# Optimization experiments

Measured on AMD Instinct MI355X. Metric: run time of the kernel, lower is better.

The kernel has to match this reference:

```python
import jax, jax.numpy as jnp
import numpy as np

N, E, NS, NB = 25000, 400000, 4, 8
S0, V0 = 64, 32            # input: 64x0e + 32x1o
MS, MV = 96, 96            # message irreps: 96x0e + 96x1o
OS, OV = 128, 32           # post-linear_down/skip: (64+64)x0e + 32x1o
NIRR = S0 + V0             # node_feats.irreps.num_irreps = 96
AVG_NEIGH = 16.0
Y1 = float(np.sqrt(3.0 / (4.0 * np.pi)))  # integral-normalized l=1 SH coeff


def setup_inputs() -> dict:
    key = jax.random.key(0)
    k = jax.random.split(key, 15)
    return {
        'node_feats': jax.random.normal(k[0], (N, S0 + 3 * V0), jnp.float32),
        'vectors': jax.random.normal(k[1], (E, 3), jnp.float32),
        'rbf': jax.random.uniform(k[2], (E, NB), jnp.float32),
        'species': jax.random.randint(k[3], (N,), 0, NS, jnp.int32),
        'senders': jax.random.randint(k[4], (E,), 0, N, jnp.int32),
        'receivers': jax.random.randint(k[5], (E,), 0, N, jnp.int32),
        'W_up_s': jax.random.normal(k[6], (S0, S0), jnp.float32),
        'W_up_v': jax.random.normal(k[7], (V0, V0), jnp.float32),
        'W_mlp1': jax.random.normal(k[8], (NB, 64), jnp.float32),
        'W_mlp2': jax.random.normal(k[9], (64, 64), jnp.float32),
        'W_mlp3': jax.random.normal(k[10], (64, MS + MV), jnp.float32),
        'W_down_s': jax.random.normal(k[11], (MS, OS), jnp.float32),
        'W_down_v': jax.random.normal(k[12], (MV, OV), jnp.float32),
        'W_skip_s': jax.random.normal(k[13], (NS, S0, OS), jnp.float32),
        'W_skip_v': jax.random.normal(k[14], (NS, V0, OV), jnp.float32),
    }


def reference(node_feats, vectors, rbf, species, senders, receivers,
              W_up_s, W_up_v, W_mlp1, W_mlp2, W_mlp3,
              W_down_s, W_down_v, W_skip_s, W_skip_v):
    n = node_feats.shape[0]
    s = node_feats[:, :S0]                      # [N, 64]   0e
    v = node_feats[:, S0:].reshape(n, V0, 3)    # [N, 32,3] 1o

    # linear_up (per-irrep linear, 1/sqrt(fan_in) path normalization), then gather
    s_up = (s @ W_up_s) * (1.0 / jnp.sqrt(S0))
    v_up = jnp.einsum('nci,cd->ndi', v, W_up_v) * (1.0 / jnp.sqrt(V0))
    s_e = s_up[senders]                         # [E, 64]
    v_e = v_up[senders]                         # [E, 32, 3]

    # spherical harmonics l=1, normalize=True, 'integral' normalization
    y = Y1 * vectors / (jnp.linalg.norm(vectors, axis=-1, keepdims=True) + 1e-12)

    # tensor products filtered to output irreps + 0e
    tp_v = s_e[:, :, None] * y[:, None, :]                       # 0e x 1o -> 1o [E,64,3]
    tp_s = jnp.einsum('eci,ei->ec', v_e, y) * (1.0 / jnp.sqrt(3.0))  # 1o x 1o -> 0e [E,32]
    msg_s = jnp.concatenate([s_e, tp_s], axis=1)                 # [E, 96]
    msg_v = jnp.concatenate([v_e, tp_v], axis=1)                 # [E, 96, 3]

    # radial MLP -> per-edge, per-irrep mixing weights
    h = jax.nn.silu(rbf @ W_mlp1 * (1.0 / jnp.sqrt(NB)))
    h = jax.nn.silu(h @ W_mlp2 * (1.0 / 8.0))
    mix = h @ W_mlp3 * (1.0 / 8.0)                               # [E, 192]

    inv = 1.0 / NIRR
    msg_s = msg_s * mix[:, :MS] * inv
    msg_v = msg_v * (mix[:, MS:] * inv)[:, :, None]

    # scatter-sum to receivers, then normalize by sqrt(avg_num_neighbors)
    agg_s = jax.ops.segment_sum(msg_s, receivers, num_segments=n) / jnp.sqrt(AVG_NEIGH)
    agg_v = jax.ops.segment_sum(msg_v, receivers, num_segments=n) / jnp.sqrt(AVG_NEIGH)

    # linear_down to 128x0e + 32x1o
    out_s = agg_s @ W_down_s * (1.0 / jnp.sqrt(MS))
    out_v = jnp.einsum('nci,cd->ndi', agg_v, W_down_v) * (1.0 / jnp.sqrt(MV))

    # species-indexed skip connection (indexed linear)
    skip_s = jnp.einsum('nc,ncd->nd', s, W_skip_s[species]) * (1.0 / jnp.sqrt(S0))
    skip_v = jnp.einsum('nci,ncd->ndi', v, W_skip_v[species]) * (1.0 / jnp.sqrt(V0))

    f_s = out_s + skip_s                                         # [N, 128]
    f_v = out_v + skip_v                                         # [N, 32, 3]

    # equivariant gate: first 96 scalars activated, last 32 scalars gate the vectors
    act_s = jax.nn.silu(f_s[:, :OS - OV])
    gates = jax.nn.silu(f_s[:, OS - OV:])
    gated_v = f_v * gates[:, :, None]
    return jnp.concatenate([act_s, gated_v.reshape(n, OV * 3)], axis=1)  # [N, 192]
```

## Files before the change

### kernel.cpp

```cpp
#include <hip/hip_runtime.h>
#include <hip/hip_bf16.h>
#include <hip/hip_fp16.h>
#include <hip/hip_fp8.h>

#define NN 25000
#define EE 400000

#define SC_UP_S 0.125f
#define SC_UP_V 0.17677669529663689f
#define Y1C 0.48860251190291992f
#define SC_MLP1 0.35355339059327373f
#define SC_MLP2 0.125f
#define SC3 0.0013020833333333333f
#define INV_SQRT3 0.57735026918962584f
#define SC_DOWN 0.025515518153991442f
#define SC_SKIP_S 0.125f
#define SC_SKIP_V 0.17677669529663689f

typedef __attribute__((ext_vector_type(8))) short short8;
typedef __attribute__((ext_vector_type(4))) float f32x4;

#if defined(__has_builtin)
#if __has_builtin(__builtin_amdgcn_cvt_pk_fp8_f32)
#define HAS_HW_FP8_ENC 1
#endif
#if __has_builtin(__builtin_amdgcn_cvt_pk_f32_fp8)
#define HAS_HW_FP8_DEC 1
#endif
#endif
#ifndef HAS_HW_FP8_ENC
#define HAS_HW_FP8_ENC 0
#endif
#ifndef HAS_HW_FP8_DEC
#define HAS_HW_FP8_DEC 0
#endif

__device__ __forceinline__ float silu(float x) {
  return __fdividef(x, 1.f + __expf(-x));
}
__device__ __forceinline__ unsigned short f2bf(float f) {
  __hip_bfloat16 h = __float2bfloat16(f);
  return *reinterpret_cast<unsigned short*>(&h);
}
__device__ __forceinline__ float bf2f(unsigned short s) {
  return __uint_as_float(((unsigned)s) << 16);
}
__device__ __forceinline__ float bfe(short8 v, int idx) {
  return __uint_as_float(((unsigned)(unsigned short)v[idx]) << 16);
}
__device__ __forceinline__ unsigned packbf(float lo, float hi) {
  return ((unsigned)f2bf(hi) << 16) | (unsigned)f2bf(lo);
}
__device__ __forceinline__ unsigned char f2fp8_sw(float x) {
  __hip_fp8_e4m3 v(x);
  return (unsigned char)v.__x;
}
__device__ __forceinline__ unsigned f2fp8x2(float a, float b) {
#if HAS_HW_FP8_ENC
  return (unsigned)__builtin_amdgcn_cvt_pk_fp8_f32(a, b, 0, false);
#else
  return (unsigned)f2fp8_sw(a) | ((unsigned)f2fp8_sw(b) << 8);
#endif
}
__device__ __forceinline__ float fp82f_sw(unsigned b) {
  __hip_fp8_e4m3 t;
  t.__x = (__hip_fp8_storage_t)b;
  return (float)t;
}
__device__ __forceinline__ void fp8x4dec(unsigned w, float* o) {
#if HAS_HW_FP8_DEC
  auto lo = __builtin_amdgcn_cvt_pk_f32_fp8((int)w, false);
  auto hi = __builtin_amdgcn_cvt_pk_f32_fp8((int)w, true);
  o[0] = lo[0]; o[1] = lo[1]; o[2] = hi[0]; o[3] = hi[1];
#else
  o[0] = fp82f_sw(w & 0xFF);
  o[1] = fp82f_sw((w >> 8) & 0xFF);
  o[2] = fp82f_sw((w >> 16) & 0xFF);
  o[3] = fp82f_sw(w >> 24);
#endif
}

#define W_W1P 0
#define W_W2P 1024
#define W_W3B 3072
#define W_WDS 9216
#define W_WDV 15360
#define W_WSS 16896
#define W_WSV 33280
#define W_SUPB 35328
#define W_VUPB (W_SUPB + NN * 32)
#define W_DEG (W_VUPB + NN * 48)
#define W_PRE (W_DEG + NN)
#define W_CUR (W_PRE + NN + 8)
#define W_RNK (W_CUR + NN)
#define W_EDN (W_RNK + EE)
#define W_END (W_EDN + EE * 56)


__global__ __launch_bounds__(256) void transpose_weights(
    const float* __restrict__ W1, const float* __restrict__ W2,
    const float* __restrict__ W3, const float* __restrict__ Wds,
    const float* __restrict__ Wdv, const float* __restrict__ Wss,
    const float* __restrict__ Wsv, float* __restrict__ ws) {
  int t = blockIdx.x * 256 + threadIdx.x;
  int stride = gridDim.x * 256;
  unsigned short* W1p = (unsigned short*)(ws + W_W1P);
  unsigned short* W2p = (unsigned short*)(ws + W_W2P);
  unsigned short* W3b = (unsigned short*)(ws + W_W3B);
  unsigned short* Wdsb = (unsigned short*)(ws + W_WDS);
  unsigned short* Wdvb = (unsigned short*)(ws + W_WDV);
  unsigned short* Wssb = (unsigned short*)(ws + W_WSS);
  unsigned short* Wsvb = (unsigned short*)(ws + W_WSV);
  for (int i = t; i < 2048; i += stride) {
    int c = i >> 5, k = i & 31;
    W1p[i] = (k < 8) ? f2bf(W1[k * 64 + c] * SC_MLP1) : (unsigned short)0;
  }
  for (int i = t; i < 4096; i += stride) {
    int c = i >> 6, k = i & 63;
    W2p[i] = f2bf(W2[k * 64 + c] * SC_MLP2);
  }
  for (int i = t; i < 12288; i += stride) {
    int c = i >> 6, k = i & 63;
    float sc = (c >= 64 && c < 96) ? (SC3 * INV_SQRT3) : SC3;
    W3b[i] = f2bf(W3[k * 192 + c] * sc);
  }
  for (int i = t; i < 12288; i += stride) {
    int o = i / 96, k = i - 96 * o;
    Wdsb[i] = f2bf(Wds[k * 128 + o] * SC_DOWN);
  }
  for (int i = t; i < 3072; i += stride) {
    int o = i / 96, k = i - 96 * o;
    Wdvb[i] = f2bf(Wdv[k * 32 + o] * SC_DOWN);
  }
  for (int i = t; i < 32768; i += stride)
    Wssb[i] = f2bf(Wss[i] * SC_SKIP_S);
  for (int i = t; i < 4096; i += stride)
    Wsvb[i] = f2bf(Wsv[i] * SC_SKIP_V);
}

__global__ __launch_bounds__(256) void up_kernel(
    const float* __restrict__ nf, const float* __restrict__ Wus,
    const float* __restrict__ Wuv, unsigned short* __restrict__ s_upb,
    unsigned short* __restrict__ v_upb) {
  int n = blockIdx.x;
  int t = threadIdx.x;
  __shared__ float sv[160];
  if (t < 160) sv[t] = nf[n * 160 + t];
  __syncthreads();
  if (t < 64) {
    float a = 0.f;
#pragma unroll
    for (int k = 0; k < 64; k++) a += sv[k] * Wus[k * 64 + t];
    s_upb[n * 64 + t] = f2bf(a * SC_UP_S);
  } else if (t < 160) {
    int j = t - 64;
    int c = j / 3, i = j - 3 * c;
    float a = 0.f;
#pragma unroll
    for (int k = 0; k < 32; k++) a += sv[64 + k * 3 + i] * Wuv[k * 32 + c];
    v_upb[n * 96 + j] = f2bf(a * SC_UP_V);
  }
}

__global__ __launch_bounds__(256) void count_deg(
    const int* __restrict__ receivers, int* __restrict__ deg) {
  int e = blockIdx.x * 256 + threadIdx.x;
  if (e < EE) atomicAdd(&deg[receivers[e]], 1);
}

__global__ __launch_bounds__(1024) void scan_kernel(
    const int* __restrict__ deg, int* __restrict__ prefix,
    int* __restrict__ cursor) {
  __shared__ int waveSums[16];
  __shared__ int sCarry;
  int t = threadIdx.x;
  int lane = t & 63, wv = t >> 6;
  if (t == 0) sCarry = 0;
  __syncthreads();
  for (int base = 0; base < NN; base += 1024) {
    int i = base + t;
    int x = (i < NN) ? deg[i] : 0;
    int v = x;
#pragma unroll
    for (int d = 1; d < 64; d <<= 1) {
      int u = __shfl_up(v, d, 64);
      if (lane >= d) v += u;
    }
    if (lane == 63) waveSums[wv] = v;
    __syncthreads();
    if (wv == 0 && lane < 16) {
      int s = waveSums[lane];
#pragma unroll
      for (int d = 1; d < 16; d <<= 1) {
        int u = __shfl_up(s, d, 64);
        if (lane >= d) s += u;
      }
      waveSums[lane] = s;
    }
    __syncthreads();
    int waveOff = (wv == 0) ? 0 : waveSums[wv - 1];
    int incl = v + waveOff + sCarry;
    if (i < NN) {
      prefix[i] = incl - x;
      cursor[i] = incl - x;
    }
    __syncthreads();
    if (t == 1023) sCarry = incl;
    __syncthreads();
  }
  if (t == 0) prefix[NN] = sCarry;
}

__global__ __launch_bounds__(256) void rank_kernel(
    const int* __restrict__ receivers, int* __restrict__ cursor,
    int* __restrict__ rankArr) {
  int e = blockIdx.x * 256 + threadIdx.x;
  if (e < EE) {
    int r = receivers[e];
    rankArr[e] = atomicAdd(&cursor[r], 1);
  }
}

__global__ __launch_bounds__(256, 4) void edge_down7(
    const float* __restrict__ rbf, const float* __restrict__ vectors,
    const int* __restrict__ senders, const int* __restrict__ rankArr,
    const unsigned short* __restrict__ W1p,
    const unsigned short* __restrict__ W2p,
    const unsigned short* __restrict__ W3b,
    const unsigned short* __restrict__ Wdsb,
    const unsigned short* __restrict__ Wdvb,
    const unsigned short* __restrict__ s_upb,
    const unsigned short* __restrict__ v_upb,
    unsigned char* __restrict__ edown) {
  __shared__ unsigned short sMix[64 * 200];
  unsigned short* sH = sMix;
  __shared__ int sRank[64];

  int t = threadIdx.x;
  int pbase = blockIdx.x * 64;
  int lane = t & 63;
  int wv = t >> 6;
  int rl = lane & 15;
  int kgrp = lane >> 4;
  int arow = 16 * wv + rl;
  int crow = 16 * wv + kgrp * 4;

  union S8 { short8 v; unsigned u[4]; };

  if (t < 64) sRank[t] = rankArr[pbase + t];
  int eid = pbase + arow;
  int snd = senders[eid];
  const unsigned short* seb = s_upb + (size_t)snd * 64;
  const unsigned short* veb = v_upb + (size_t)snd * 96;
  short8 se0 = *(const short8*)&seb[kgrp * 8];
  short8 se1 = *(const short8*)&seb[32 + kgrp * 8];
  short8 ve0 = *(const short8*)&veb[24 * kgrp];
  short8 ve1 = *(const short8*)&veb[24 * kgrp + 8];
  short8 ve2 = *(const short8*)&veb[24 * kgrp + 16];
  float vx = vectors[(size_t)eid * 3 + 0];
  float vy = vectors[(size_t)eid * 3 + 1];
  float vz = vectors[(size_t)eid * 3 + 2];
  float nrm = sqrtf(vx * vx + vy * vy + vz * vz) + 1e-12f;
  float ysc = Y1C / nrm;
  float y0 = vx * ysc, y1 = vy * ysc, y2 = vz * ysc;

  S8 a1;
  a1.u[0] = a1.u[1] = a1.u[2] = a1.u[3] = 0u;
  if (kgrp == 0) {
    float4 ra = *(const float4*)(rbf + (size_t)eid * 8);
    float4 rb = *(const float4*)(rbf + (size_t)eid * 8 + 4);
    a1.u[0] = packbf(ra.x, ra.y);
    a1.u[1] = packbf(ra.z, ra.w);
    a1.u[2] = packbf(rb.x, rb.y);
    a1.u[3] = packbf(rb.z, rb.w);
  }
#pragma unroll
  for (int ct = 0; ct < 4; ct++) {
    short8 b = *(const short8*)&W1p[(ct * 16 + rl) * 32 + kgrp * 8];
    f32x4 acc = {0.f, 0.f, 0.f, 0.f};
    acc = __builtin_amdgcn_mfma_f32_16x16x32_bf16(a1.v, b, acc, 0, 0, 0);
#pragma unroll
    for (int rr = 0; rr < 4; rr++)
      sH[(crow + rr) * 72 + ct * 16 + rl] = f2bf(silu(acc[rr]));
  }

  {
    short8 a20 = *(const short8*)&sH[arow * 72 + kgrp * 8];
    short8 a21 = *(const short8*)&sH[arow * 72 + 32 + kgrp * 8];
    short8 b0s[4], b1s[4];
#pragma unroll
    for (int ct = 0; ct < 4; ct++) {
      const unsigned short* wb = &W2p[(ct * 16 + rl) * 64];
      b0s[ct] = *(const short8*)&wb[kgrp * 8];
      b1s[ct] = *(const short8*)&wb[32 + kgrp * 8];
    }
#pragma unroll
    for (int ct = 0; ct < 4; ct++) {
      f32x4 acc = {0.f, 0.f, 0.f, 0.f};
      acc = __builtin_amdgcn_mfma_f32_16x16x32_bf16(a20, b0s[ct], acc, 0, 0, 0);
      acc = __builtin_amdgcn_mfma_f32_16x16x32_bf16(a21, b1s[ct], acc, 0, 0, 0);
#pragma unroll
      for (int rr = 0; rr < 4; rr++)
        sH[(crow + rr) * 72 + ct * 16 + rl] = f2bf(silu(acc[rr]));
    }
  }

  short8 a30 = *(const short8*)&sH[arow * 72 + kgrp * 8];
  short8 a31 = *(const short8*)&sH[arow * 72 + 32 + kgrp * 8];
  __syncthreads();
  {
#pragma unroll
    for (int half = 0; half < 2; half++) {
      short8 b0s[6], b1s[6];
#pragma unroll
      for (int j = 0; j < 6; j++) {
        int cc = (half * 6 + j) * 16 + rl;
        const unsigned short* wb = &W3b[cc * 64];
        b0s[j] = *(const short8*)&wb[kgrp * 8];
        b1s[j] = *(const short8*)&wb[32 + kgrp * 8];
      }
#pragma unroll
      for (int j = 0; j < 6; j++) {
        int cc = (half * 6 + j) * 16 + rl;
        f32x4 acc = {0.f, 0.f, 0.f, 0.f};
        acc = __builtin_amdgcn_mfma_f32_16x16x32_bf16(a30, b0s[j], acc, 0, 0, 0);
        acc = __builtin_amdgcn_mfma_f32_16x16x32_bf16(a31, b1s[j], acc, 0, 0, 0);
#pragma unroll
        for (int rr = 0; rr < 4; rr++)
          sMix[(crow + rr) * 200 + cc] = f2bf(acc[rr]);
      }
    }
  }

  const unsigned short* mrow = &sMix[arow * 200];
  S8 as0, as1, as2, mvp1, mvp2, mvp3;
  {
    short8 m = *(const short8*)&mrow[kgrp * 8];
#pragma unroll
    for (int q = 0; q < 4; q++)
      as0.u[q] = packbf(bfe(se0, 2 * q) * bfe(m, 2 * q),
                        bfe(se0, 2 * q + 1) * bfe(m, 2 * q + 1));
  }
  {
    short8 m = *(const short8*)&mrow[32 + kgrp * 8];
#pragma unroll
    for (int q = 0; q < 4; q++)
      as1.u[q] = packbf(bfe(se1, 2 * q) * bfe(m, 2 * q),
                        bfe(se1, 2 * q + 1) * bfe(m, 2 * q + 1));
  }
  {
    short8 m = *(const short8*)&mrow[64 + kgrp * 8];
#pragma unroll
    for (int q = 0; q < 4; q++) {
      float e0, e1, e2, f0, f1, f2;
      if (6 * q < 8) e0 = bfe(ve0, 6 * q); else if (6 * q < 16) e0 = bfe(ve1, 6 * q - 8); else e0 = bfe(ve2, 6 * q - 16);
      if (6 * q + 1 < 8) e1 = bfe(ve0, 6 * q + 1); else if (6 * q + 1 < 16) e1 = bfe(ve1, 6 * q - 7); else e1 = bfe(ve2, 6 * q - 15);
      if (6 * q + 2 < 8) e2 = bfe(ve0, 6 * q + 2); else if (6 * q + 2 < 16) e2 = bfe(ve1, 6 * q - 6); else e2 = bfe(ve2, 6 * q - 14);
      if (6 * q + 3 < 8) f0 = bfe(ve0, 6 * q + 3); else if (6 * q + 3 < 16) f0 = bfe(ve1, 6 * q - 5); else f0 = bfe(ve2, 6 * q - 13);
      if (6 * q + 4 < 8) f1 = bfe(ve0, 6 * q + 4); else if (6 * q + 4 < 16) f1 = bfe(ve1, 6 * q - 4); else f1 = bfe(ve2, 6 * q - 12);
      if (6 * q + 5 < 8) f2 = bfe(ve0, 6 * q + 5); else if (6 * q + 5 < 16) f2 = bfe(ve1, 6 * q - 3); else f2 = bfe(ve2, 6 * q - 11);
      float da = e0 * y0 + e1 * y1 + e2 * y2;
      float db = f0 * y0 + f1 * y1 + f2 * y2;
      as2.u[q] = packbf(da * bfe(m, 2 * q), db * bfe(m, 2 * q + 1));
    }
  }
  mvp1.v = *(const short8*)&mrow[96 + kgrp * 8];
  mvp2.v = *(const short8*)&mrow[128 + kgrp * 8];
  mvp3.v = *(const short8*)&mrow[160 + kgrp * 8];
  __syncthreads();

  unsigned char* edL = (unsigned char*)sMix;
#pragma unroll
  for (int half = 0; half < 2; half++) {
    short8 b0s[4], b1s[4], b2s[4];
#pragma unroll
    for (int j = 0; j < 4; j++) {
      int col = (half * 4 + j) * 16 + rl;
      const unsigned short* wb = &Wdsb[col * 96];
      b0s[j] = *(const short8*)&wb[kgrp * 8];
      b1s[j] = *(const short8*)&wb[32 + kgrp * 8];
      b2s[j] = *(const short8*)&wb[64 + kgrp * 8];
    }
#pragma unroll
    for (int j = 0; j < 4; j++) {
      int col = (half * 4 + j) * 16 + rl;
      f32x4 acc = {0.f, 0.f, 0.f, 0.f};
      acc = __builtin_amdgcn_mfma_f32_16x16x32_bf16(as0.v, b0s[j], acc, 0, 0, 0);
      acc = __builtin_amdgcn_mfma_f32_16x16x32_bf16(as1.v, b1s[j], acc, 0, 0, 0);
      acc = __builtin_amdgcn_mfma_f32_16x16x32_bf16(as2.v, b2s[j], acc, 0, 0, 0);
      unsigned p01 = f2fp8x2(acc[0], acc[1]);
      unsigned p23 = f2fp8x2(acc[2], acc[3]);
      edL[(crow + 0) * 232 + col] = (unsigned char)p01;
      edL[(crow + 1) * 232 + col] = (unsigned char)(p01 >> 8);
      edL[(crow + 2) * 232 + col] = (unsigned char)p23;
      edL[(crow + 3) * 232 + col] = (unsigned char)(p23 >> 8);
    }
  }
  float yarr[3] = {y0, y1, y2};
#pragma unroll
  for (int i = 0; i < 3; i++) {
    S8 av0, av1, av2;
#pragma unroll
    for (int q = 0; q < 4; q++) {
      float g0, g1;
      int ja = 6 * q + i, jb = 6 * q + 3 + i;
      if (ja < 8) g0 = bfe(ve0, ja); else if (ja < 16) g0 = bfe(ve1, ja - 8); else g0 = bfe(ve2, ja - 16);
      if (jb < 8) g1 = bfe(ve0, jb); else if (jb < 16) g1 = bfe(ve1, jb - 8); else g1 = bfe(ve2, jb - 16);
      av0.u[q] = packbf(g0 * bfe(mvp1.v, 2 * q), g1 * bfe(mvp1.v, 2 * q + 1));
      av1.u[q] = packbf(bfe(se0, 2 * q) * yarr[i] * bfe(mvp2.v, 2 * q),
                        bfe(se0, 2 * q + 1) * yarr[i] * bfe(mvp2.v, 2 * q + 1));
      av2.u[q] = packbf(bfe(se1, 2 * q) * yarr[i] * bfe(mvp3.v, 2 * q),
                        bfe(se1, 2 * q + 1) * yarr[i] * bfe(mvp3.v, 2 * q + 1));
    }
#pragma unroll
    for (int ot = 0; ot < 2; ot++) {
      int o = ot * 16 + rl;
      const unsigned short* wb = &Wdvb[o * 96];
      short8 b0 = *(const short8*)&wb[kgrp * 8];
      short8 b1 = *(const short8*)&wb[32 + kgrp * 8];
      short8 b2 = *(const short8*)&wb[64 + kgrp * 8];
      f32x4 acc = {0.f, 0.f, 0.f, 0.f};
      acc = __builtin_amdgcn_mfma_f32_16x16x32_bf16(av0.v, b0, acc, 0, 0, 0);
      acc = __builtin_amdgcn_mfma_f32_16x16x32_bf16(av1.v, b1, acc, 0, 0, 0);
      acc = __builtin_amdgcn_mfma_f32_16x16x32_bf16(av2.v, b2, acc, 0, 0, 0);
      unsigned p01 = f2fp8x2(acc[0], acc[1]);
      unsigned p23 = f2fp8x2(acc[2], acc[3]);
      edL[(crow + 0) * 232 + 128 + o * 3 + i] = (unsigned char)p01;
      edL[(crow + 1) * 232 + 128 + o * 3 + i] = (unsigned char)(p01 >> 8);
      edL[(crow + 2) * 232 + 128 + o * 3 + i] = (unsigned char)p23;
      edL[(crow + 3) * 232 + 128 + o * 3 + i] = (unsigned char)(p23 >> 8);
    }
  }
  __syncthreads();

  {
    int row = t >> 2, q = t & 3;
    const unsigned* src = (const unsigned*)(edL + row * 232 + q * 56);
    unsigned* dst = (unsigned*)(edown + (size_t)sRank[row] * 224 + q * 56);
#pragma unroll
    for (int j = 0; j < 14; j++) dst[j] = src[j];
  }
}

__global__ __launch_bounds__(256) void gather_out4(
    const float* __restrict__ nf, const int* __restrict__ species,
    const int* __restrict__ prefix, const unsigned char* __restrict__ edown,
    const unsigned short* __restrict__ Wssb,
    const unsigned short* __restrict__ Wsvb, float* __restrict__ out) {
  int n = blockIdx.x;
  int t = threadIdx.x;
  __shared__ float sNF[160];
  __shared__ float sPart[16 * 224];
  __shared__ float sEd[224];
  __shared__ float sF[224];
  if (t < 160) sNF[t] = nf[(size_t)n * 160 + t];
  int beg = prefix[n], end = prefix[n + 1];
  if (t < 224) {
    int u = t % 14, rg = t / 14;
    float a[16];
#pragma unroll
    for (int j = 0; j < 16; j++) a[j] = 0.f;
    for (int s = beg + rg; s < end; s += 16) {
      uint4 v = *(const uint4*)(edown + (size_t)s * 224 + u * 16);
      float d[4];
      fp8x4dec(v.x, d);
      a[0] += d[0]; a[1] += d[1]; a[2] += d[2]; a[3] += d[3];
      fp8x4dec(v.y, d);
      a[4] += d[0]; a[5] += d[1]; a[6] += d[2]; a[7] += d[3];
      fp8x4dec(v.z, d);
      a[8] += d[0]; a[9] += d[1]; a[10] += d[2]; a[11] += d[3];
      fp8x4dec(v.w, d);
      a[12] += d[0]; a[13] += d[1]; a[14] += d[2]; a[15] += d[3];
    }
#pragma unroll
    for (int j = 0; j < 16; j += 4)
      *(float4*)&sPart[rg * 224 + u * 16 + j] = *(float4*)&a[j];
  }
  __syncthreads();
  if (t < 224) {
    float s = 0.f;
#pragma unroll
    for (int rg = 0; rg < 16; rg++) s += sPart[rg * 224 + t];
    sEd[t] = s;
  }
  __syncthreads();
  int spec = species[n];
  if (t < 128) {
    const unsigned short* wsk = Wssb + (size_t)spec * 8192;
    float b = 0.f;
#pragma unroll
    for (int k = 0; k < 64; k++) b += sNF[k] * bf2f(wsk[k * 128 + t]);
    sF[t] = sEd[t] + b;
  } else if (t < 224) {
    int j = t - 128;
    int c = j / 3, i = j - 3 * c;
    const unsigned short* wsk = Wsvb + (size_t)spec * 1024;
    float b = 0.f;
#pragma unroll
    for (int k = 0; k < 32; k++) b += sNF[64 + k * 3 + i] * bf2f(wsk[k * 32 + c]);
    sF[t] = sEd[t] + b;
  }
  __syncthreads();
  if (t < 96) {
    out[(size_t)n * 192 + t] = silu(sF[t]);
  } else if (t < 192) {
    int j = t - 96;
    int c = j / 3;
    out[(size_t)n * 192 + t] = sF[128 + j] * silu(sF[96 + c]);
  }
}

extern "C" void kernel_launch(void* const* d_in, const int* in_sizes, int n_in,
                              void* d_out, int out_size, void* d_ws, size_t ws_size,
                              hipStream_t stream) {
  const float* nf = (const float*)d_in[0];
  const float* vectors = (const float*)d_in[1];
  const float* rbf = (const float*)d_in[2];
  const int* species = (const int*)d_in[3];
  const int* senders = (const int*)d_in[4];
  const int* receivers = (const int*)d_in[5];
  const float* Wus = (const float*)d_in[6];
  const float* Wuv = (const float*)d_in[7];
  const float* W1 = (const float*)d_in[8];
  const float* W2 = (const float*)d_in[9];
  const float* W3 = (const float*)d_in[10];
  const float* Wds = (const float*)d_in[11];
  const float* Wdv = (const float*)d_in[12];
  const float* Wss = (const float*)d_in[13];
  const float* Wsv = (const float*)d_in[14];

  float* ws = (float*)d_ws;
  const unsigned short* W1p = (const unsigned short*)(ws + W_W1P);
  const unsigned short* W2p = (const unsigned short*)(ws + W_W2P);
  const unsigned short* W3b = (const unsigned short*)(ws + W_W3B);
  const unsigned short* Wdsb = (const unsigned short*)(ws + W_WDS);
  const unsigned short* Wdvb = (const unsigned short*)(ws + W_WDV);
  const unsigned short* Wssb = (const unsigned short*)(ws + W_WSS);
  const unsigned short* Wsvb = (const unsigned short*)(ws + W_WSV);
  unsigned short* s_upb = (unsigned short*)(ws + W_SUPB);
  unsigned short* v_upb = (unsigned short*)(ws + W_VUPB);
  int* deg = (int*)(ws + W_DEG);
  int* prefix = (int*)(ws + W_PRE);
  int* cursor = (int*)(ws + W_CUR);
  int* rankArr = (int*)(ws + W_RNK);
  unsigned char* edown = (unsigned char*)(ws + W_EDN);
  float* out = (float*)d_out;

  transpose_weights<<<16, 256, 0, stream>>>(W1, W2, W3, Wds, Wdv, Wss, Wsv, ws);
  up_kernel<<<NN, 256, 0, stream>>>(nf, Wus, Wuv, s_upb, v_upb);

  hipMemsetAsync(deg, 0, (size_t)NN * sizeof(int), stream);
  count_deg<<<(EE + 255) / 256, 256, 0, stream>>>(receivers, deg);
  scan_kernel<<<1, 1024, 0, stream>>>(deg, prefix, cursor);
  rank_kernel<<<(EE + 255) / 256, 256, 0, stream>>>(receivers, cursor, rankArr);
  edge_down7<<<EE / 64, 256, 0, stream>>>(rbf, vectors, senders, rankArr, W1p,
                                          W2p, W3b, Wdsb, Wdvb, s_upb, v_upb,
                                          edown);
  gather_out4<<<NN, 256, 0, stream>>>(nf, species, prefix, edown, Wssb, Wsvb,
                                      out);
}
```

Before: 349.3 us.

## Write edge outputs in edge order and gather via sorted edge-id indirection

Instead of scattering each edge's fp8 message row to its receiver-sorted rank position, the edge kernel now writes rows contiguously in edge order. The counting-sort pass stores a sorted edge-id list, and the gather kernel reads through it. This turns scattered 224-byte writes into coalesced ones, at the cost of random 16-byte reads plus an extra index load per edge in the gather.

```diff
diff --git a/kernel.cpp b/kernel.cpp
--- a/kernel.cpp
+++ b/kernel.cpp
@@ -92,8 +92,8 @@
 #define W_DEG (W_VUPB + NN * 48)
 #define W_PRE (W_DEG + NN)
 #define W_CUR (W_PRE + NN + 8)
-#define W_RNK (W_CUR + NN)
-#define W_EDN (W_RNK + EE)
+#define W_SEID (W_CUR + NN)
+#define W_EDN (W_SEID + EE)
 #define W_END (W_EDN + EE * 56)
 
 
@@ -211,19 +211,20 @@
   if (t == 0) prefix[NN] = sCarry;
 }
 
-__global__ __launch_bounds__(256) void rank_kernel(
+__global__ __launch_bounds__(256) void scatter_eid(
     const int* __restrict__ receivers, int* __restrict__ cursor,
-    int* __restrict__ rankArr) {
+    int* __restrict__ sortedEid) {
   int e = blockIdx.x * 256 + threadIdx.x;
   if (e < EE) {
     int r = receivers[e];
-    rankArr[e] = atomicAdd(&cursor[r], 1);
-  }
-}
-
-__global__ __launch_bounds__(256, 4) void edge_down7(
+    int pos = atomicAdd(&cursor[r], 1);
+    sortedEid[pos] = e;
+  }
+}
+
+__global__ __launch_bounds__(256, 4) void edge_down8(
     const float* __restrict__ rbf, const float* __restrict__ vectors,
-    const int* __restrict__ senders, const int* __restrict__ rankArr,
+    const int* __restrict__ senders,
     const unsigned short* __restrict__ W1p,
     const unsigned short* __restrict__ W2p,
     const unsigned short* __restrict__ W3b,
@@ -234,7 +235,6 @@
     unsigned char* __restrict__ edown) {
   __shared__ unsigned short sMix[64 * 200];
   unsigned short* sH = sMix;
-  __shared__ int sRank[64];
 
   int t = threadIdx.x;
   int pbase = blockIdx.x * 64;
@@ -247,7 +247,6 @@
 
   union S8 { short8 v; unsigned u[4]; };
 
-  if (t < 64) sRank[t] = rankArr[pbase + t];
   int eid = pbase + arow;
   int snd = senders[eid];
   const unsigned short* seb = s_upb + (size_t)snd * 64;
@@ -436,15 +435,16 @@
   {
     int row = t >> 2, q = t & 3;
     const unsigned* src = (const unsigned*)(edL + row * 232 + q * 56);
-    unsigned* dst = (unsigned*)(edown + (size_t)sRank[row] * 224 + q * 56);
+    unsigned* dst = (unsigned*)(edown + (size_t)(pbase + row) * 224 + q * 56);
 #pragma unroll
     for (int j = 0; j < 14; j++) dst[j] = src[j];
   }
 }
 
-__global__ __launch_bounds__(256) void gather_out4(
+__global__ __launch_bounds__(256) void gather_out6(
     const float* __restrict__ nf, const int* __restrict__ species,
-    const int* __restrict__ prefix, const unsigned char* __restrict__ edown,
+    const int* __restrict__ prefix, const int* __restrict__ sortedEid,
+    const unsigned char* __restrict__ edown,
     const unsigned short* __restrict__ Wssb,
     const unsigned short* __restrict__ Wsvb, float* __restrict__ out) {
   int n = blockIdx.x;
@@ -461,7 +461,8 @@
 #pragma unroll
     for (int j = 0; j < 16; j++) a[j] = 0.f;
     for (int s = beg + rg; s < end; s += 16) {
-      uint4 v = *(const uint4*)(edown + (size_t)s * 224 + u * 16);
+      int e = sortedEid[s];
+      uint4 v = *(const uint4*)(edown + (size_t)e * 224 + u * 16);
       float d[4];
       fp8x4dec(v.x, d);
       a[0] += d[0]; a[1] += d[1]; a[2] += d[2]; a[3] += d[3];
@@ -542,7 +543,7 @@
   int* deg = (int*)(ws + W_DEG);
   int* prefix = (int*)(ws + W_PRE);
   int* cursor = (int*)(ws + W_CUR);
-  int* rankArr = (int*)(ws + W_RNK);
+  int* sortedEid = (int*)(ws + W_SEID);
   unsigned char* edown = (unsigned char*)(ws + W_EDN);
   float* out = (float*)d_out;
 
@@ -552,10 +553,10 @@
   hipMemsetAsync(deg, 0, (size_t)NN * sizeof(int), stream);
   count_deg<<<(EE + 255) / 256, 256, 0, stream>>>(receivers, deg);
   scan_kernel<<<1, 1024, 0, stream>>>(deg, prefix, cursor);
-  rank_kernel<<<(EE + 255) / 256, 256, 0, stream>>>(receivers, cursor, rankArr);
-  edge_down7<<<EE / 64, 256, 0, stream>>>(rbf, vectors, senders, rankArr, W1p,
-                                          W2p, W3b, Wdsb, Wdvb, s_upb, v_upb,
-                                          edown);
-  gather_out4<<<NN, 256, 0, stream>>>(nf, species, prefix, edown, Wssb, Wsvb,
-                                      out);
-}
+  scatter_eid<<<(EE + 255) / 256, 256, 0, stream>>>(receivers, cursor,
+                                                    sortedEid);
+  edge_down8<<<EE / 64, 256, 0, stream>>>(rbf, vectors, senders, W1p, W2p, W3b,
+                                          Wdsb, Wdvb, s_upb, v_upb, edown);
+  gather_out6<<<NN, 256, 0, stream>>>(nf, species, prefix, sortedEid, edown,
+                                      Wssb, Wsvb, out);
+}
```

After: 355.0 us. About the same (+1.6%).
